# Optimization experiments

Hardware: AMD Instinct MI355X
Metric: run time of the kernel (lower is better)

Reference implementation:

```python
import jax, jax.numpy as jnp
import numpy as np

N = 40000   # nodes
E = 640000  # edges (before self-loops)
G = 64      # graphs
EPS = 1e-5


def _gat_conv(x, src, dst, W, a_src, a_dst, bias, n_nodes):
    """PyG GATConv, heads=1, leaky_relu slope 0.2, with self-loops already in src/dst."""
    h = x @ W.T                              # [N, out]
    s_score = h @ a_src                      # [N]
    d_score = h @ a_dst                      # [N]
    e = jax.nn.leaky_relu(s_score[src] + d_score[dst], 0.2)  # [E]
    m = jax.ops.segment_max(e, dst, num_segments=n_nodes)
    ex = jnp.exp(e - m[dst])
    z = jax.ops.segment_sum(ex, dst, num_segments=n_nodes)
    alpha = ex / z[dst]                      # per-dst softmax over incoming edges
    out = jax.ops.segment_sum(h[src] * alpha[:, None], dst, num_segments=n_nodes)
    return out + bias


def _layer_norm(x, gamma, beta):
    mu = jnp.mean(x, axis=-1, keepdims=True)
    var = jnp.mean((x - mu) ** 2, axis=-1, keepdims=True)
    return gamma * (x - mu) * jax.lax.rsqrt(var + EPS) + beta


def setup_inputs() -> dict:
    key = jax.random.key(0)
    ks = jax.random.split(key, 16)
    x = jax.random.normal(ks[0], (N, 128), dtype=jnp.float32)
    edge_index = jax.random.randint(ks[1], (2, E), 0, N, dtype=jnp.int32)
    batch = jnp.sort(jax.random.randint(ks[2], (N,), 0, G, dtype=jnp.int32))
    def glorot(k, shape):
        fan = shape[-1]
        return jax.random.normal(k, shape, dtype=jnp.float32) / jnp.sqrt(jnp.float32(fan))
    return {
        "x": x, "edge_index": edge_index, "batch": batch,
        "W1": glorot(ks[3], (128, 128)), "a1_src": glorot(ks[4], (128,)),
        "a1_dst": glorot(ks[5], (128,)), "b1": jnp.zeros((128,), jnp.float32),
        "g1": jnp.ones((128,), jnp.float32), "be1": jnp.zeros((128,), jnp.float32),
        "W2": glorot(ks[6], (64, 128)), "a2_src": glorot(ks[7], (64,)),
        "a2_dst": glorot(ks[8], (64,)), "b2": jnp.zeros((64,), jnp.float32),
        "g2": jnp.ones((64,), jnp.float32), "be2": jnp.zeros((64,), jnp.float32),
        "Wl": glorot(ks[9], (64, 64)), "bl": jnp.zeros((64,), jnp.float32),
        "Wc": glorot(ks[10], (1, 64)), "bc": jnp.zeros((1,), jnp.float32),
    }


def reference(x, edge_index, batch, W1, a1_src, a1_dst, b1, g1, be1,
              W2, a2_src, a2_dst, b2, g2, be2, Wl, bl, Wc, bc):
    # add self-loops as PyG GATConv does by default
    loops = jnp.arange(N, dtype=edge_index.dtype)
    src = jnp.concatenate([edge_index[0], loops])
    dst = jnp.concatenate([edge_index[1], loops])

    h = jax.nn.relu(_gat_conv(x, src, dst, W1, a1_src, a1_dst, b1, N))
    h = _layer_norm(h, g1, be1)
    h = jax.nn.relu(_gat_conv(h, src, dst, W2, a2_src, a2_dst, b2, N))
    h = _layer_norm(h, g2, be2)

    # global mean pool over graphs
    sums = jax.ops.segment_sum(h, batch, num_segments=G)          # [G, 64]
    cnt = jax.ops.segment_sum(jnp.ones((N,), h.dtype), batch, num_segments=G)
    pooled = sums / jnp.maximum(cnt, 1.0)[:, None]

    out = pooled @ Wl.T + bl
    out = out @ Wc.T + bc                                          # [G, 1]
    return out.squeeze(-1)                                         # [G]
```

## Files before the change

kernel.cpp:

```cpp
#include <hip/hip_runtime.h>
#include <hip/hip_fp16.h>
#include <math.h>

#define NNODES 40000
#define NEDGES 640000
#define NGRAPH 64
#define CAP 96
constexpr float LN_EPS = 1e-5f;


typedef _Float16 v8h __attribute__((ext_vector_type(8)));
typedef float    v4f __attribute__((ext_vector_type(4)));

__device__ __forceinline__ float bf_sum(float v) {
    #pragma unroll
    for (int o = 32; o > 0; o >>= 1) v += __shfl_xor(v, o);
    return v;
}

__global__ void bin_prep(const int* __restrict__ ei, int E,
                         int* __restrict__ cnt, unsigned short* __restrict__ ssrc,
                         const float* __restrict__ W1, const float* __restrict__ W2,
                         _Float16* __restrict__ Bf1, _Float16* __restrict__ Bf2,
                         float* __restrict__ sums) {
    const int t = blockIdx.x * blockDim.x + threadIdx.x;
    if (t < 128 * 128) {
        const int o = t >> 7, k = t & 127;
        const int nt = o >> 4, lc = o & 15;
        const int ks = k >> 5, g = (k >> 3) & 3, j = k & 7;
        Bf1[(size_t)(((nt * 4 + ks) * 64 + g * 16 + lc) * 8 + j)] = (_Float16)W1[t];
    }
    if (t < 64 * 128) {
        const int o = t >> 7, k = t & 127;
        const int nt = o >> 4, lc = o & 15;
        const int ks = k >> 5, g = (k >> 3) & 3, j = k & 7;
        Bf2[(size_t)(((nt * 4 + ks) * 64 + g * 16 + lc) * 8 + j)] = (_Float16)W2[t];
    }
    if (t < NGRAPH * 64) sums[t] = 0.f;
    if (t < E) {
        const int s = ei[t], d = ei[E + t];
        const int pos = atomicAdd(cnt + d, 1);
        if (pos < CAP) ssrc[d * CAP + pos] = (unsigned short)s;
    }
}

template<int DOUT, bool F16IN>
__global__ __launch_bounds__(256) void gemm_scores_mfma(
        const void* __restrict__ Xin, const _Float16* __restrict__ Bfrag,
        const float* __restrict__ asrc, const float* __restrict__ adst,
        __half* __restrict__ H, float* __restrict__ S, float* __restrict__ Dv) {
    constexpr int NT = DOUT / 16;
    __shared__ _Float16 xs[64][136];
    const int tid = threadIdx.x;
    const int base = blockIdx.x * 64;

    if (F16IN) {
        const _Float16* Xh = (const _Float16*)Xin;
        for (int c = tid; c < 64 * 16; c += 256) {
            const int row = c >> 4, c8 = c & 15;
            *(float4*)&xs[row][c8 * 8] =
                *(const float4*)(Xh + (size_t)(base + row) * 128 + c8 * 8);
        }
    } else {
        const float* Xf = (const float*)Xin;
        for (int c = tid; c < 64 * 32; c += 256) {
            const int row = c >> 5, c4 = c & 31;
            const float4 v = *(const float4*)(Xf + (size_t)(base + row) * 128 + c4 * 4);
            _Float16 h4[4] = {(_Float16)v.x, (_Float16)v.y, (_Float16)v.z, (_Float16)v.w};
            *(uint2*)&xs[row][c4 * 4] = *(const uint2*)h4;
        }
    }
    __syncthreads();

    const int lane = tid & 63;
    const int wv   = tid >> 6;
    const int nb   = base + wv * 16;
    const int lc = lane & 15, g = lane >> 4;

    v8h a[4];
    #pragma unroll
    for (int ks = 0; ks < 4; ++ks)
        a[ks] = *(const v8h*)&xs[wv * 16 + lc][ks * 32 + g * 8];

    v4f acc[NT];
    #pragma unroll
    for (int nt = 0; nt < NT; ++nt) acc[nt] = (v4f){0.f, 0.f, 0.f, 0.f};

    #pragma unroll
    for (int ks = 0; ks < 4; ++ks) {
        #pragma unroll
        for (int nt = 0; nt < NT; ++nt) {
            const v8h bv = *(const v8h*)(Bfrag + (size_t)(((nt * 4 + ks) * 64 + lane) * 8));
            acc[nt] = __builtin_amdgcn_mfma_f32_16x16x32_f16(a[ks], bv, acc[nt], 0, 0, 0);
        }
    }

    float sp[4] = {0.f, 0.f, 0.f, 0.f}, dp[4] = {0.f, 0.f, 0.f, 0.f};
    #pragma unroll
    for (int nt = 0; nt < NT; ++nt) {
        const float as_ = asrc[nt * 16 + lc];
        const float ad_ = adst[nt * 16 + lc];
        #pragma unroll
        for (int r = 0; r < 4; ++r) {
            const float hv = acc[nt][r];
            H[(size_t)(nb + g * 4 + r) * DOUT + nt * 16 + lc] = __float2half_rn(hv);
            sp[r] += hv * as_;
            dp[r] += hv * ad_;
        }
    }
    #pragma unroll
    for (int o = 8; o > 0; o >>= 1) {
        #pragma unroll
        for (int r = 0; r < 4; ++r) {
            sp[r] += __shfl_xor(sp[r], o);
            dp[r] += __shfl_xor(dp[r], o);
        }
    }
    #pragma unroll
    for (int r = 0; r < 4; ++r) {
        if (lc == r) {
            S[nb + g * 4 + r]  = sp[r];
            Dv[nb + g * 4 + r] = dp[r];
        }
    }
}

template<int D>
__device__ __forceinline__ void aggr_one_generic(
        const int node, const int deg, const int lane,
        const unsigned short* __restrict__ ssrc, const float* __restrict__ S,
        const float dsc, const __half* __restrict__ H,
        float& acc0, float& acc1, float& z) {
    constexpr int VPL = D / 64;
    float zz = 0.f;
    const int r0 = node * CAP;
    for (int bse = 0; bse < deg; bse += 64) {
        const int n = min(64, deg - bse);
        int s = 0; float a = 0.f;
        if (lane < n) {
            s = ssrc[r0 + bse + lane];
            float t = S[s] + dsc;
            t = t > 0.f ? t : 0.2f * t;
            a = __expf(t);
        }
        zz += bf_sum(a);
        const int abits = __float_as_int(a);
        for (int j = 0; j < n; ++j) {
            const int sj = __builtin_amdgcn_readlane(s, j);
            const float aj = __int_as_float(__builtin_amdgcn_readlane(abits, j));
            const __half* hp = H + (size_t)sj * D;
            if (VPL == 1) {
                acc0 += aj * __half2float(hp[lane]);
            } else {
                const float2 f = __half22float2(*(const __half2*)(hp + 2 * lane));
                acc0 += aj * f.x; acc1 += aj * f.y;
            }
        }
    }
    z = zz;
}

template<int D, int POOL>
__device__ __forceinline__ void finish_node(
        const int node, const int lane,
        float acc0, float acc1, float z, const float aself, const float2 selfF,
        const float* __restrict__ b, const float* __restrict__ gam,
        const float* __restrict__ bet,
        __half* __restrict__ outh, const int* __restrict__ batch,
        float* __restrict__ sums) {
    constexpr int VPL = D / 64;
    acc0 += aself * selfF.x;
    if (VPL == 2) acc1 += aself * selfF.y;
    z += aself;
    const float zinv = 1.0f / z;
    float vv[VPL], lsum = 0.f;
    vv[0] = acc0;
    if (VPL == 2) vv[1] = acc1;
    #pragma unroll
    for (int k = 0; k < VPL; ++k) {
        const int ch = VPL * lane + k;
        vv[k] = fmaxf(vv[k] * zinv + b[ch], 0.f);
        lsum += vv[k];
    }
    const float mu = bf_sum(lsum) / D;
    float q = 0.f;
    #pragma unroll
    for (int k = 0; k < VPL; ++k) { vv[k] -= mu; q += vv[k] * vv[k]; }
    const float rstd = rsqrtf(bf_sum(q) / D + LN_EPS);
    #pragma unroll
    for (int k = 0; k < VPL; ++k) {
        const int ch = VPL * lane + k;
        vv[k] = gam[ch] * vv[k] * rstd + bet[ch];
    }
    if (POOL) {
        const int bg = batch[node];
        atomicAdd(&sums[bg * D + lane], vv[0]);
    } else {
        if (VPL == 2)
            *(__half2*)(outh + (size_t)node * D + 2 * lane) =
                __floats2half2_rn(vv[0], vv[1]);
        else
            outh[(size_t)node * D + lane] = __float2half_rn(vv[0]);
    }
}

template<int D, int POOL>
__global__ __launch_bounds__(256) void gat_aggr(
        const int* __restrict__ cnt, const unsigned short* __restrict__ ssrc,
        const float* __restrict__ S, const float* __restrict__ Dv,
        const __half* __restrict__ H,
        const float* __restrict__ b, const float* __restrict__ gam,
        const float* __restrict__ bet,
        __half* __restrict__ outh, const int* __restrict__ batch,
        float* __restrict__ sums) {
    constexpr int VPL = D / 64;
    const int lane = threadIdx.x & 63;
    const int wv   = threadIdx.x >> 6;
    const int nodeA = blockIdx.x * 8 + wv * 2;
    const int nodeB = nodeA + 1;

    const int degA = min(__builtin_amdgcn_readfirstlane(cnt[nodeA]), CAP);
    const int degB = min(__builtin_amdgcn_readfirstlane(cnt[nodeB]), CAP);
    const float dscA = Dv[nodeA], dscB = Dv[nodeB];

    float tsA = S[nodeA] + dscA; tsA = tsA > 0.f ? tsA : 0.2f * tsA;
    float tsB = S[nodeB] + dscB; tsB = tsB > 0.f ? tsB : 0.2f * tsB;
    const float aselfA = __expf(tsA);
    const float aselfB = __expf(tsB);

    float2 selfFA, selfFB;
    if (VPL == 1) {
        selfFA = make_float2(__half2float(H[(size_t)nodeA * D + lane]), 0.f);
        selfFB = make_float2(__half2float(H[(size_t)nodeB * D + lane]), 0.f);
    } else {
        selfFA = __half22float2(*(const __half2*)(H + (size_t)nodeA * D + 2 * lane));
        selfFB = __half22float2(*(const __half2*)(H + (size_t)nodeB * D + 2 * lane));
    }

    float accA0 = 0.f, accA1 = 0.f, accB0 = 0.f, accB1 = 0.f;
    float zA, zB;

    if (degA <= 64 && degB <= 64) {
        int sA = 0, sB = 0;
        if (lane < degA) sA = ssrc[nodeA * CAP + lane];
        if (lane < degB) sB = ssrc[nodeB * CAP + lane];
        float tA = S[sA] + dscA;
        float tB = S[sB] + dscB;
        tA = tA > 0.f ? tA : 0.2f * tA;
        tB = tB > 0.f ? tB : 0.2f * tB;
        const float aA = (lane < degA) ? __expf(tA) : 0.f;
        const float aB = (lane < degB) ? __expf(tB) : 0.f;
        zA = bf_sum(aA);
        zB = bf_sum(aB);
        const int abA = __float_as_int(aA), abB = __float_as_int(aB);

        const int nmA = (degA + 7) & ~7;
        const int nmB = (degB + 7) & ~7;
        const int nmax = max(nmA, nmB);
        for (int j = 0; j < nmax; j += 8) {
            const bool doA = j < nmA, doB = j < nmB;
            float afA[8], afB[8];
            __half2 hvA[8], hvB[8];
            __half hsA[8], hsB[8];
            if (doA) {
                #pragma unroll
                for (int u = 0; u < 8; ++u) {
                    const int sj = __builtin_amdgcn_readlane(sA, j + u);
                    afA[u] = __int_as_float(__builtin_amdgcn_readlane(abA, j + u));
                    const __half* hp = H + (size_t)sj * D;
                    if (VPL == 1) hsA[u] = hp[lane];
                    else          hvA[u] = *(const __half2*)(hp + 2 * lane);
                }
            }
            if (doB) {
                #pragma unroll
                for (int u = 0; u < 8; ++u) {
                    const int sj = __builtin_amdgcn_readlane(sB, j + u);
                    afB[u] = __int_as_float(__builtin_amdgcn_readlane(abB, j + u));
                    const __half* hp = H + (size_t)sj * D;
                    if (VPL == 1) hsB[u] = hp[lane];
                    else          hvB[u] = *(const __half2*)(hp + 2 * lane);
                }
            }
            if (doA) {
                #pragma unroll
                for (int u = 0; u < 8; ++u) {
                    if (VPL == 1) {
                        accA0 += afA[u] * __half2float(hsA[u]);
                    } else {
                        accA0 += afA[u] * __half2float(__low2half(hvA[u]));
                        accA1 += afA[u] * __half2float(__high2half(hvA[u]));
                    }
                }
            }
            if (doB) {
                #pragma unroll
                for (int u = 0; u < 8; ++u) {
                    if (VPL == 1) {
                        accB0 += afB[u] * __half2float(hsB[u]);
                    } else {
                        accB0 += afB[u] * __half2float(__low2half(hvB[u]));
                        accB1 += afB[u] * __half2float(__high2half(hvB[u]));
                    }
                }
            }
        }
    } else {
        aggr_one_generic<D>(nodeA, degA, lane, ssrc, S, dscA, H, accA0, accA1, zA);
        aggr_one_generic<D>(nodeB, degB, lane, ssrc, S, dscB, H, accB0, accB1, zB);
    }

    finish_node<D, POOL>(nodeA, lane, accA0, accA1, zA, aselfA, selfFA,
                         b, gam, bet, outh, batch, sums);
    finish_node<D, POOL>(nodeB, lane, accB0, accB1, zB, aselfB, selfFB,
                         b, gam, bet, outh, batch, sums);
}

__global__ void final_head(const float* __restrict__ sums, const int* __restrict__ batch,
                           const float* __restrict__ Wl, const float* __restrict__ bl,
                           const float* __restrict__ Wc, const float* __restrict__ bc,
                           float* __restrict__ out) {
    __shared__ float p[64];
    __shared__ float red[64];
    const int g = blockIdx.x, tid = threadIdx.x;
    int lo = 0, hi = NNODES;
    while (lo < hi) { int mid = (lo + hi) >> 1; if (batch[mid] < g) lo = mid + 1; else hi = mid; }
    int lo2 = lo, hi2 = NNODES;
    while (lo2 < hi2) { int mid = (lo2 + hi2) >> 1; if (batch[mid] < g + 1) lo2 = mid + 1; else hi2 = mid; }
    const float cnt = (float)(lo2 - lo);
    p[tid] = sums[g * 64 + tid] / fmaxf(cnt, 1.0f);
    __syncthreads();
    float t = bl[tid];
    #pragma unroll 8
    for (int k = 0; k < 64; ++k) t += Wl[tid * 64 + k] * p[k];
    red[tid] = Wc[tid] * t;
    __syncthreads();
    for (int s = 32; s > 0; s >>= 1) {
        if (tid < s) red[tid] += red[tid + s];
        __syncthreads();
    }
    if (tid == 0) out[g] = red[0] + bc[0];
}

extern "C" void kernel_launch(void* const* d_in, const int* in_sizes, int n_in,
                              void* d_out, int out_size, void* d_ws, size_t ws_size,
                              hipStream_t stream) {
    const int N = NNODES, E = NEDGES, G = NGRAPH;

    const float* x      = (const float*)d_in[0];
    const int*   ei     = (const int*)d_in[1];
    const int*   batch  = (const int*)d_in[2];
    const float* W1     = (const float*)d_in[3];
    const float* a1s    = (const float*)d_in[4];
    const float* a1d    = (const float*)d_in[5];
    const float* b1     = (const float*)d_in[6];
    const float* g1     = (const float*)d_in[7];
    const float* be1    = (const float*)d_in[8];
    const float* W2     = (const float*)d_in[9];
    const float* a2s    = (const float*)d_in[10];
    const float* a2d    = (const float*)d_in[11];
    const float* b2     = (const float*)d_in[12];
    const float* g2     = (const float*)d_in[13];
    const float* be2    = (const float*)d_in[14];
    const float* Wl     = (const float*)d_in[15];
    const float* bl     = (const float*)d_in[16];
    const float* Wc     = (const float*)d_in[17];
    const float* bc     = (const float*)d_in[18];

    char* w = (char*)d_ws;
    __half* h1   = (__half*)w; w += (size_t)N * 128 * 2;
    __half* v1h  = (__half*)w; w += (size_t)N * 128 * 2;
    __half* h2   = (__half*)w; w += (size_t)N * 64 * 2;
    float* S1    = (float*)w; w += (size_t)N * 4;
    float* Dv1   = (float*)w; w += (size_t)N * 4;
    float* S2    = (float*)w; w += (size_t)N * 4;
    float* Dv2   = (float*)w; w += (size_t)N * 4;
    int* cnt     = (int*)w;   w += (size_t)N * 4;
    unsigned short* ssrc = (unsigned short*)w; w += (size_t)N * CAP * 2;
    _Float16* Bf1 = (_Float16*)w; w += (size_t)128 * 128 * 2;
    _Float16* Bf2 = (_Float16*)w; w += (size_t)64 * 128 * 2;
    float* sums  = (float*)w; w += (size_t)G * 64 * 4;

    const int TB = 256;

    hipMemsetAsync(cnt, 0, (size_t)N * 4, stream);
    bin_prep<<<(E + TB - 1) / TB, TB, 0, stream>>>(ei, E, cnt, ssrc, W1, W2,
                                                   Bf1, Bf2, sums);

    gemm_scores_mfma<128, false><<<N / 64, 256, 0, stream>>>(x, Bf1, a1s, a1d,
                                                             h1, S1, Dv1);

    gat_aggr<128, 0><<<N / 8, 256, 0, stream>>>(cnt, ssrc, S1, Dv1, h1, b1, g1, be1,
                                                v1h, nullptr, nullptr);

    gemm_scores_mfma<64, true><<<N / 64, 256, 0, stream>>>(v1h, Bf2, a2s, a2d,
                                                           h2, S2, Dv2);

    gat_aggr<64, 1><<<N / 8, 256, 0, stream>>>(cnt, ssrc, S2, Dv2, h2, b2, g2, be2,
                                               nullptr, batch, sums);

    final_head<<<G, 64, 0, stream>>>(sums, batch, Wl, bl, Wc, bc, (float*)d_out);
}
```

Measured before the change: 243.8 us.

## Fuse final head into pooling aggregation via last-block counter and LDS pre-reduction

Removes the separate final_head launch by having the last block to finish the layer-2 aggregation compute the pooled MLP head, using a global atomic counter reset in bin_prep. Node contributions to the graph sums are pre-reduced in shared memory per block when they belong to the block's first graph, which cuts global atomics. The two nodes' wave reductions are also interleaved (bf_sum2) to overlap shuffle latency. This adds __syncthreads, threadfences and a serial tail done by a single block.

```diff
diff --git a/kernel.cpp b/kernel.cpp
--- a/kernel.cpp
+++ b/kernel.cpp
@@ -17,13 +17,21 @@
     for (int o = 32; o > 0; o >>= 1) v += __shfl_xor(v, o);
     return v;
 }
+__device__ __forceinline__ void bf_sum2(float& a, float& b) {
+    #pragma unroll
+    for (int o = 32; o > 0; o >>= 1) {
+        a += __shfl_xor(a, o);
+        b += __shfl_xor(b, o);
+    }
+}
 
 __global__ void bin_prep(const int* __restrict__ ei, int E,
                          int* __restrict__ cnt, unsigned short* __restrict__ ssrc,
                          const float* __restrict__ W1, const float* __restrict__ W2,
                          _Float16* __restrict__ Bf1, _Float16* __restrict__ Bf2,
-                         float* __restrict__ sums) {
+                         float* __restrict__ sums, int* __restrict__ ctr) {
     const int t = blockIdx.x * blockDim.x + threadIdx.x;
+    if (t == 0) *ctr = 0;
     if (t < 128 * 128) {
         const int o = t >> 7, k = t & 127;
         const int nt = o >> 4, lc = o & 15;
@@ -160,47 +168,46 @@
     z = zz;
 }
 
-template<int D, int POOL>
-__device__ __forceinline__ void finish_node(
-        const int node, const int lane,
-        float acc0, float acc1, float z, const float aself, const float2 selfF,
+template<int D>
+__device__ __forceinline__ void ln_pair(
+        float accA0, float accA1, float zA, const float aselfA, const float2 sfA,
+        float accB0, float accB1, float zB, const float aselfB, const float2 sfB,
+        const int lane,
         const float* __restrict__ b, const float* __restrict__ gam,
-        const float* __restrict__ bet,
-        __half* __restrict__ outh, const int* __restrict__ batch,
-        float* __restrict__ sums) {
+        const float* __restrict__ bet, float vA[2], float vB[2]) {
     constexpr int VPL = D / 64;
-    acc0 += aself * selfF.x;
-    if (VPL == 2) acc1 += aself * selfF.y;
-    z += aself;
-    const float zinv = 1.0f / z;
-    float vv[VPL], lsum = 0.f;
-    vv[0] = acc0;
-    if (VPL == 2) vv[1] = acc1;
-    #pragma unroll
-    for (int k = 0; k < VPL; ++k) {
-        const int ch = VPL * lane + k;
-        vv[k] = fmaxf(vv[k] * zinv + b[ch], 0.f);
-        lsum += vv[k];
-    }
-    const float mu = bf_sum(lsum) / D;
-    float q = 0.f;
-    #pragma unroll
-    for (int k = 0; k < VPL; ++k) { vv[k] -= mu; q += vv[k] * vv[k]; }
-    const float rstd = rsqrtf(bf_sum(q) / D + LN_EPS);
-    #pragma unroll
-    for (int k = 0; k < VPL; ++k) {
-        const int ch = VPL * lane + k;
-        vv[k] = gam[ch] * vv[k] * rstd + bet[ch];
-    }
-    if (POOL) {
-        const int bg = batch[node];
-        atomicAdd(&sums[bg * D + lane], vv[0]);
-    } else {
-        if (VPL == 2)
-            *(__half2*)(outh + (size_t)node * D + 2 * lane) =
-                __floats2half2_rn(vv[0], vv[1]);
-        else
-            outh[(size_t)node * D + lane] = __float2half_rn(vv[0]);
+    accA0 += aselfA * sfA.x; accB0 += aselfB * sfB.x;
+    if (VPL == 2) { accA1 += aselfA * sfA.y; accB1 += aselfB * sfB.y; }
+    zA += aselfA; zB += aselfB;
+    const float ziA = 1.0f / zA, ziB = 1.0f / zB;
+    const int ch0 = VPL * lane;
+    float lsA, lsB;
+    vA[0] = fmaxf(accA0 * ziA + b[ch0], 0.f);
+    vB[0] = fmaxf(accB0 * ziB + b[ch0], 0.f);
+    lsA = vA[0]; lsB = vB[0];
+    if (VPL == 2) {
+        vA[1] = fmaxf(accA1 * ziA + b[ch0 + 1], 0.f);
+        vB[1] = fmaxf(accB1 * ziB + b[ch0 + 1], 0.f);
+        lsA += vA[1]; lsB += vB[1];
+    }
+    bf_sum2(lsA, lsB);
+    const float muA = lsA / D, muB = lsB / D;
+    float qA, qB;
+    vA[0] -= muA; qA = vA[0] * vA[0];
+    vB[0] -= muB; qB = vB[0] * vB[0];
+    if (VPL == 2) {
+        vA[1] -= muA; qA += vA[1] * vA[1];
+        vB[1] -= muB; qB += vB[1] * vB[1];
+    }
+    bf_sum2(qA, qB);
+    const float rsA = rsqrtf(qA / D + LN_EPS), rsB = rsqrtf(qB / D + LN_EPS);
+    const float g0 = gam[ch0], e0 = bet[ch0];
+    vA[0] = g0 * vA[0] * rsA + e0;
+    vB[0] = g0 * vB[0] * rsB + e0;
+    if (VPL == 2) {
+        const float g1 = gam[ch0 + 1], e1 = bet[ch0 + 1];
+        vA[1] = g1 * vA[1] * rsA + e1;
+        vB[1] = g1 * vB[1] * rsB + e1;
     }
 }
 
@@ -212,8 +219,20 @@
         const float* __restrict__ b, const float* __restrict__ gam,
         const float* __restrict__ bet,
         __half* __restrict__ outh, const int* __restrict__ batch,
-        float* __restrict__ sums) {
+        float* __restrict__ sums, int* __restrict__ ctr,
+        const float* __restrict__ Wl, const float* __restrict__ bl,
+        const float* __restrict__ Wc, const float* __restrict__ bc,
+        float* __restrict__ out) {
     constexpr int VPL = D / 64;
+    __shared__ float psum[64];
+    __shared__ int pbg;
+    __shared__ int lastFlag;
+    if (POOL) {
+        if (threadIdx.x == 0) pbg = batch[blockIdx.x * 8];
+        if (threadIdx.x < 64) psum[threadIdx.x] = 0.f;
+        __syncthreads();
+    }
+
     const int lane = threadIdx.x & 63;
     const int wv   = threadIdx.x >> 6;
     const int nodeA = blockIdx.x * 8 + wv * 2;
@@ -250,8 +269,8 @@
         tB = tB > 0.f ? tB : 0.2f * tB;
         const float aA = (lane < degA) ? __expf(tA) : 0.f;
         const float aB = (lane < degB) ? __expf(tB) : 0.f;
-        zA = bf_sum(aA);
-        zB = bf_sum(aB);
+        zA = aA; zB = aB;
+        bf_sum2(zA, zB);
         const int abA = __float_as_int(aA), abB = __float_as_int(aB);
 
         const int nmA = (degA + 7) & ~7;
@@ -310,36 +329,51 @@
         aggr_one_generic<D>(nodeB, degB, lane, ssrc, S, dscB, H, accB0, accB1, zB);
     }
 
-    finish_node<D, POOL>(nodeA, lane, accA0, accA1, zA, aselfA, selfFA,
-                         b, gam, bet, outh, batch, sums);
-    finish_node<D, POOL>(nodeB, lane, accB0, accB1, zB, aselfB, selfFB,
-                         b, gam, bet, outh, batch, sums);
-}
-
-__global__ void final_head(const float* __restrict__ sums, const int* __restrict__ batch,
-                           const float* __restrict__ Wl, const float* __restrict__ bl,
-                           const float* __restrict__ Wc, const float* __restrict__ bc,
-                           float* __restrict__ out) {
-    __shared__ float p[64];
-    __shared__ float red[64];
-    const int g = blockIdx.x, tid = threadIdx.x;
-    int lo = 0, hi = NNODES;
-    while (lo < hi) { int mid = (lo + hi) >> 1; if (batch[mid] < g) lo = mid + 1; else hi = mid; }
-    int lo2 = lo, hi2 = NNODES;
-    while (lo2 < hi2) { int mid = (lo2 + hi2) >> 1; if (batch[mid] < g + 1) lo2 = mid + 1; else hi2 = mid; }
-    const float cnt = (float)(lo2 - lo);
-    p[tid] = sums[g * 64 + tid] / fmaxf(cnt, 1.0f);
-    __syncthreads();
-    float t = bl[tid];
-    #pragma unroll 8
-    for (int k = 0; k < 64; ++k) t += Wl[tid * 64 + k] * p[k];
-    red[tid] = Wc[tid] * t;
-    __syncthreads();
-    for (int s = 32; s > 0; s >>= 1) {
-        if (tid < s) red[tid] += red[tid + s];
+    float vA[2], vB[2];
+    ln_pair<D>(accA0, accA1, zA, aselfA, selfFA,
+               accB0, accB1, zB, aselfB, selfFB,
+               lane, b, gam, bet, vA, vB);
+
+    if (!POOL) {
+        if (VPL == 2) {
+            *(__half2*)(outh + (size_t)nodeA * D + 2 * lane) = __floats2half2_rn(vA[0], vA[1]);
+            *(__half2*)(outh + (size_t)nodeB * D + 2 * lane) = __floats2half2_rn(vB[0], vB[1]);
+        } else {
+            outh[(size_t)nodeA * D + lane] = __float2half_rn(vA[0]);
+            outh[(size_t)nodeB * D + lane] = __float2half_rn(vB[0]);
+        }
+    } else {
+        const int bgA = batch[nodeA], bgB = batch[nodeB];
+        const int pb = pbg;
+        if (bgA == pb) atomicAdd(&psum[lane], vA[0]);
+        else           atomicAdd(&sums[bgA * 64 + lane], vA[0]);
+        if (bgB == pb) atomicAdd(&psum[lane], vB[0]);
+        else           atomicAdd(&sums[bgB * 64 + lane], vB[0]);
         __syncthreads();
-    }
-    if (tid == 0) out[g] = red[0] + bc[0];
+        if (threadIdx.x < 64) atomicAdd(&sums[pb * 64 + threadIdx.x], psum[threadIdx.x]);
+        __threadfence();
+        __syncthreads();
+        if (threadIdx.x == 0)
+            lastFlag = (atomicAdd(ctr, 1) == (int)gridDim.x - 1);
+        __syncthreads();
+
+        if (lastFlag) {
+            for (int g0 = 0; g0 < NGRAPH; g0 += 4) {
+                const int g = g0 + wv;
+                int lo = 0, hi = NNODES;
+                while (lo < hi) { int m = (lo + hi) >> 1; if (batch[m] < g) lo = m + 1; else hi = m; }
+                int lo2 = lo, hi2 = NNODES;
+                while (lo2 < hi2) { int m = (lo2 + hi2) >> 1; if (batch[m] < g + 1) lo2 = m + 1; else hi2 = m; }
+                const float c = fmaxf((float)(lo2 - lo), 1.0f);
+                const float pv = atomicAdd(&sums[g * 64 + lane], 0.f) / c;
+                float t = bl[lane];
+                for (int k = 0; k < 64; ++k)
+                    t += Wl[lane * 64 + k] * __shfl(pv, k);
+                const float r = bf_sum(Wc[lane] * t);
+                if (lane == 0) out[g] = r + bc[0];
+            }
+        }
+    }
 }
 
 extern "C" void kernel_launch(void* const* d_in, const int* in_sizes, int n_in,
@@ -380,24 +414,26 @@
     _Float16* Bf1 = (_Float16*)w; w += (size_t)128 * 128 * 2;
     _Float16* Bf2 = (_Float16*)w; w += (size_t)64 * 128 * 2;
     float* sums  = (float*)w; w += (size_t)G * 64 * 4;
+    int* ctr     = (int*)w;  w += 64;
 
     const int TB = 256;
 
     hipMemsetAsync(cnt, 0, (size_t)N * 4, stream);
     bin_prep<<<(E + TB - 1) / TB, TB, 0, stream>>>(ei, E, cnt, ssrc, W1, W2,
-                                                   Bf1, Bf2, sums);
+                                                   Bf1, Bf2, sums, ctr);
 
     gemm_scores_mfma<128, false><<<N / 64, 256, 0, stream>>>(x, Bf1, a1s, a1d,
                                                              h1, S1, Dv1);
 
     gat_aggr<128, 0><<<N / 8, 256, 0, stream>>>(cnt, ssrc, S1, Dv1, h1, b1, g1, be1,
-                                                v1h, nullptr, nullptr);
+                                                v1h, nullptr, nullptr, nullptr,
+                                                nullptr, nullptr, nullptr, nullptr,
+                                                nullptr);
 
     gemm_scores_mfma<64, true><<<N / 64, 256, 0, stream>>>(v1h, Bf2, a2s, a2d,
                                                            h2, S2, Dv2);
 
     gat_aggr<64, 1><<<N / 8, 256, 0, stream>>>(cnt, ssrc, S2, Dv2, h2, b2, g2, be2,
-                                               nullptr, batch, sums);
-
-    final_head<<<G, 64, 0, stream>>>(sums, batch, Wl, bl, Wc, bc, (float*)d_out);
-}
+                                               nullptr, batch, sums, ctr,
+                                               Wl, bl, Wc, bc, (float*)d_out);
+}
```

Measured after the change: 666.6 us. +173.4%, slower.

## Fuse edge binning into layer-1 GEMM launch and drop memset

Applied to the files above, without the earlier changes.

Edge binning by destination moves out of the prep kernel and into extra blocks of the first GEMM/score kernel, so binning and the GEMM run concurrently in one launch. The memset of the per-node counters is replaced by zeroing inside a small prep kernel that also converts the weights. This cuts one launch and one memset and lets the atomic-heavy binning overlap with the MFMA GEMM. In exchange the grid is heterogeneous and the two workloads share the GPU inside one kernel.

```diff
diff --git a/kernel.cpp b/kernel.cpp
--- a/kernel.cpp
+++ b/kernel.cpp
@@ -18,12 +18,12 @@
     return v;
 }
 
-__global__ void bin_prep(const int* __restrict__ ei, int E,
-                         int* __restrict__ cnt, unsigned short* __restrict__ ssrc,
-                         const float* __restrict__ W1, const float* __restrict__ W2,
-                         _Float16* __restrict__ Bf1, _Float16* __restrict__ Bf2,
-                         float* __restrict__ sums) {
-    const int t = blockIdx.x * blockDim.x + threadIdx.x;
+__global__ void prep_small(int* __restrict__ cnt,
+                           const float* __restrict__ W1, const float* __restrict__ W2,
+                           _Float16* __restrict__ Bf1, _Float16* __restrict__ Bf2,
+                           float* __restrict__ sums) {
+    const int t = blockIdx.x * 256 + threadIdx.x;
+    if (t < NNODES) cnt[t] = 0;
     if (t < 128 * 128) {
         const int o = t >> 7, k = t & 127;
         const int nt = o >> 4, lc = o & 15;
@@ -37,10 +37,99 @@
         Bf2[(size_t)(((nt * 4 + ks) * 64 + g * 16 + lc) * 8 + j)] = (_Float16)W2[t];
     }
     if (t < NGRAPH * 64) sums[t] = 0.f;
-    if (t < E) {
-        const int s = ei[t], d = ei[E + t];
-        const int pos = atomicAdd(cnt + d, 1);
-        if (pos < CAP) ssrc[d * CAP + pos] = (unsigned short)s;
+}
+
+template<int DOUT, bool F16IN, int NGB>
+__global__ __launch_bounds__(256) void gemm_scores_bin(
+        const void* __restrict__ Xin, const _Float16* __restrict__ Bfrag,
+        const float* __restrict__ asrc, const float* __restrict__ adst,
+        __half* __restrict__ H, float* __restrict__ S, float* __restrict__ Dv,
+        const int* __restrict__ ei, int E,
+        int* __restrict__ cnt, unsigned short* __restrict__ ssrc) {
+    constexpr int NT = DOUT / 16;
+    __shared__ _Float16 xs[64][136];
+    const int tid = threadIdx.x;
+
+    if (blockIdx.x >= NGB) {
+        const int e = (blockIdx.x - NGB) * 256 + tid;
+        if (e < E) {
+            const int s = ei[e], d = ei[E + e];
+            const int pos = atomicAdd(cnt + d, 1);
+            if (pos < CAP) ssrc[d * CAP + pos] = (unsigned short)s;
+        }
+        return;
+    }
+
+    const int base = blockIdx.x * 64;
+
+    if (F16IN) {
+        const _Float16* Xh = (const _Float16*)Xin;
+        for (int c = tid; c < 64 * 16; c += 256) {
+            const int row = c >> 4, c8 = c & 15;
+            *(float4*)&xs[row][c8 * 8] =
+                *(const float4*)(Xh + (size_t)(base + row) * 128 + c8 * 8);
+        }
+    } else {
+        const float* Xf = (const float*)Xin;
+        for (int c = tid; c < 64 * 32; c += 256) {
+            const int row = c >> 5, c4 = c & 31;
+            const float4 v = *(const float4*)(Xf + (size_t)(base + row) * 128 + c4 * 4);
+            _Float16 h4[4] = {(_Float16)v.x, (_Float16)v.y, (_Float16)v.z, (_Float16)v.w};
+            *(uint2*)&xs[row][c4 * 4] = *(const uint2*)h4;
+        }
+    }
+    __syncthreads();
+
+    const int lane = tid & 63;
+    const int wv   = tid >> 6;
+    const int nb   = base + wv * 16;
+    const int lc = lane & 15, g = lane >> 4;
+
+    v8h a[4];
+    #pragma unroll
+    for (int ks = 0; ks < 4; ++ks)
+        a[ks] = *(const v8h*)&xs[wv * 16 + lc][ks * 32 + g * 8];
+
+    v4f acc[NT];
+    #pragma unroll
+    for (int nt = 0; nt < NT; ++nt) acc[nt] = (v4f){0.f, 0.f, 0.f, 0.f};
+
+    #pragma unroll
+    for (int ks = 0; ks < 4; ++ks) {
+        #pragma unroll
+        for (int nt = 0; nt < NT; ++nt) {
+            const v8h bv = *(const v8h*)(Bfrag + (size_t)(((nt * 4 + ks) * 64 + lane) * 8));
+            acc[nt] = __builtin_amdgcn_mfma_f32_16x16x32_f16(a[ks], bv, acc[nt], 0, 0, 0);
+        }
+    }
+
+    float sp[4] = {0.f, 0.f, 0.f, 0.f}, dp[4] = {0.f, 0.f, 0.f, 0.f};
+    #pragma unroll
+    for (int nt = 0; nt < NT; ++nt) {
+        const float as_ = asrc[nt * 16 + lc];
+        const float ad_ = adst[nt * 16 + lc];
+        #pragma unroll
+        for (int r = 0; r < 4; ++r) {
+            const float hv = acc[nt][r];
+            H[(size_t)(nb + g * 4 + r) * DOUT + nt * 16 + lc] = __float2half_rn(hv);
+            sp[r] += hv * as_;
+            dp[r] += hv * ad_;
+        }
+    }
+    #pragma unroll
+    for (int o = 8; o > 0; o >>= 1) {
+        #pragma unroll
+        for (int r = 0; r < 4; ++r) {
+            sp[r] += __shfl_xor(sp[r], o);
+            dp[r] += __shfl_xor(dp[r], o);
+        }
+    }
+    #pragma unroll
+    for (int r = 0; r < 4; ++r) {
+        if (lc == r) {
+            S[nb + g * 4 + r]  = sp[r];
+            Dv[nb + g * 4 + r] = dp[r];
+        }
     }
 }
 
@@ -381,14 +470,12 @@
     _Float16* Bf2 = (_Float16*)w; w += (size_t)64 * 128 * 2;
     float* sums  = (float*)w; w += (size_t)G * 64 * 4;
 
-    const int TB = 256;
-
-    hipMemsetAsync(cnt, 0, (size_t)N * 4, stream);
-    bin_prep<<<(E + TB - 1) / TB, TB, 0, stream>>>(ei, E, cnt, ssrc, W1, W2,
-                                                   Bf1, Bf2, sums);
-
-    gemm_scores_mfma<128, false><<<N / 64, 256, 0, stream>>>(x, Bf1, a1s, a1d,
-                                                             h1, S1, Dv1);
+    prep_small<<<(N + 255) / 256, 256, 0, stream>>>(cnt, W1, W2, Bf1, Bf2, sums);
+
+    constexpr int NGB1 = NNODES / 64;
+    const int NBB = (E + 255) / 256;
+    gemm_scores_bin<128, false, NGB1><<<NGB1 + NBB, 256, 0, stream>>>(
+        x, Bf1, a1s, a1d, h1, S1, Dv1, ei, E, cnt, ssrc);
 
     gat_aggr<128, 0><<<N / 8, 256, 0, stream>>>(cnt, ssrc, S1, Dv1, h1, b1, g1, be1,
                                                 v1h, nullptr, nullptr);
```

Measured after the change: 226.4 us. 1.08x faster.
